# Optimization experiments

Hardware: AMD Instinct MI355X
Metric: run time of the kernel (lower is better)

## Reference

```python
import jax, jax.numpy as jnp
import numpy as np

MAX_DEPTH = 9
HIDDEN = 64
EMB = 64
POS_FREQS = 6
IN_C = 1
SIZES = [4 ** d for d in range(MAX_DEPTH + 1)]
OFFSETS = np.concatenate([[0], np.cumsum(SIZES)])  # per-depth slices into concatenated node arrays
TOTAL = int(OFFSETS[-1])  # 349525
POS_DIM = 3 + 2 * POS_FREQS * 3  # 39


def _interleave(v):
    v = v & 0xFFFF
    v = (v | (v << 8)) & 0x00FF00FF
    v = (v | (v << 4)) & 0x0F0F0F0F
    v = (v | (v << 2)) & 0x33333333
    v = (v | (v << 1)) & 0x55555555
    return v


def _deinterleave(v):
    v = v & 0x55555555
    v = (v | (v >> 1)) & 0x33333333
    v = (v | (v >> 2)) & 0x0F0F0F0F
    v = (v | (v >> 4)) & 0x00FF00FF
    v = (v | (v >> 8)) & 0x0000FFFF
    return v


def _xy(d):
    keys = jnp.arange(4 ** d, dtype=jnp.int32)  # full tree: sorted Morton keys = arange
    return _deinterleave(keys), _deinterleave(keys >> 1)


def _neighbors(d):
    # [N, 9] neighbor indices in Morton order grid; -1 outside the image (matches quadtree.neighs padding)
    ix, iy = _xy(d)
    res = 1 << d
    cols = []
    for dy in (-1, 0, 1):
        for dx in (-1, 0, 1):
            nx, ny = ix + dx, iy + dy
            valid = (nx >= 0) & (nx < res) & (ny >= 0) & (ny < res)
            key = _interleave(nx) | (_interleave(ny) << 1)
            cols.append(jnp.where(valid, key, -1))
    return jnp.stack(cols, axis=1)


def _pos_enc(d):
    # node_centers_from_keys + fourier_encode
    ix, iy = _xy(d)
    res = float(1 << d)
    x = (ix.astype(jnp.float32) + 0.5) / res
    y = (iy.astype(jnp.float32) + 0.5) / res
    dn = jnp.full_like(x, float(d) / float(MAX_DEPTH))
    pos = jnp.stack([x, y, dn], axis=1)  # [N, 3]
    freqs = 2.0 ** jnp.arange(POS_FREQS, dtype=jnp.float32)
    ang = pos[:, :, None] * (2.0 * np.pi) * freqs  # [N, 3, F]
    enc = jnp.concatenate([jnp.sin(ang), jnp.cos(ang)], axis=-1).reshape(pos.shape[0], -1)  # [N, 3*2F]
    return jnp.concatenate([pos, enc], axis=1)  # [N, 39]


def setup_inputs() -> dict:
    key = jax.random.key(0)
    ks = jax.random.split(key, 10)
    s = 0.05
    return {
        "features_in": jax.random.normal(ks[0], (TOTAL, IN_C), jnp.float32),
        "in_proj_W": jax.random.normal(ks[1], (IN_C + POS_DIM, HIDDEN), jnp.float32) * s,
        "in_proj_b": jnp.zeros((HIDDEN,), jnp.float32),
        "conv_W": jax.random.normal(ks[2], (MAX_DEPTH + 1, 9 * HIDDEN, HIDDEN), jnp.float32) * s,
        "conv_b": jnp.zeros((MAX_DEPTH + 1, HIDDEN), jnp.float32),
        "emb_W": jax.random.normal(ks[3], (MAX_DEPTH + 1, HIDDEN, EMB), jnp.float32) * s,
        "emb_b": jnp.zeros((MAX_DEPTH + 1, EMB), jnp.float32),
        "ln_g": jnp.ones((MAX_DEPTH + 1, EMB), jnp.float32),
        "ln_b": jnp.zeros((MAX_DEPTH + 1, EMB), jnp.float32),
        "depth_gain": jnp.ones((MAX_DEPTH + 1,), jnp.float32),
    }


def reference(features_in, in_proj_W, in_proj_b, conv_W, conv_b, emb_W, emb_b, ln_g, ln_b, depth_gain):
    D = MAX_DEPTH
    # per-depth input projection with fourier positional encoding
    h = []
    for d in range(D + 1):
        f = features_in[OFFSETS[d]:OFFSETS[d + 1]]
        x = jnp.concatenate([f, _pos_enc(d)], axis=1)  # [N_d, in_c + 39]
        h.append(x @ in_proj_W + in_proj_b)
    # bottom-up: QuadPool (mean over 4 children; full tree => children of parent i are 4i..4i+3) + QuadConv
    for d in range(D, 0, -1):
        Np = 4 ** (d - 1)
        pooled = h[d].reshape(Np, 4, HIDDEN).mean(axis=1)
        hd1 = h[d - 1] + pooled
        if d - 1 >= 1:
            neigh = _neighbors(d - 1)  # [N, 9], -1 at borders
            N = neigh.shape[0]
            padded = jnp.concatenate([hd1, jnp.zeros((1, HIDDEN), hd1.dtype)], axis=0)
            gi = jnp.where(neigh < 0, N, neigh)
            col = padded[gi].reshape(N, 9 * HIDDEN)
            hd1 = jax.nn.relu(col @ conv_W[d - 1] + conv_b[d - 1])
        h[d - 1] = hd1
    # per-depth embedding head: Linear -> LayerNorm -> depth gain
    outs = []
    eps = 1e-5
    for d in range(D + 1):
        z = h[d] @ emb_W[d] + emb_b[d]
        mu = z.mean(-1, keepdims=True)
        var = ((z - mu) ** 2).mean(-1, keepdims=True)
        z = (z - mu) / jnp.sqrt(var + eps) * ln_g[d] + ln_b[d]
        outs.append(depth_gain[d] * z)
    return jnp.concatenate(outs, axis=0)  # [TOTAL, EMB] (E[0]..E[max_depth] concatenated)
```

## Files before the change

### kernel.cpp

```cpp
#include <hip/hip_runtime.h>
#include <hip/hip_bf16.h>

static constexpr int TOTAL = 349525;
static constexpr int OFFS[11] = {0,1,5,21,85,341,1365,5461,21845,87381,349525};
static constexpr size_t CONV_USH = (size_t)8*9*2*4*64*8;
static constexpr size_t EMB_USH  = (size_t)10*2*4*64*8;
static constexpr size_t FRAG_USH = CONV_USH + EMB_USH;
static constexpr size_t FRAG_BYTES = FRAG_USH*2*2;
static constexpr size_t HPRE_BYTES = (size_t)(87381-85)*64*4;
static constexpr int WPREP_BLOCKS = 164;
static constexpr int INPROJ_BLOCKS = (TOTAL + 127)/128;

typedef __attribute__((ext_vector_type(8))) short short8;
typedef __attribute__((ext_vector_type(4))) float f32x4;

__device__ __forceinline__ unsigned deint(unsigned v){
  v &= 0x55555555u;
  v = (v | (v>>1)) & 0x33333333u;
  v = (v | (v>>2)) & 0x0F0F0F0Fu;
  v = (v | (v>>4)) & 0x00FF00FFu;
  v = (v | (v>>8)) & 0x0000FFFFu;
  return v;
}
__device__ __forceinline__ unsigned ileave(unsigned v){
  v &= 0xFFFFu;
  v = (v | (v<<8)) & 0x00FF00FFu;
  v = (v | (v<<4)) & 0x0F0F0F0Fu;
  v = (v | (v<<2)) & 0x33333333u;
  v = (v | (v<<1)) & 0x55555555u;
  return v;
}
__device__ __forceinline__ unsigned short f2bh(float x){
  unsigned u = __float_as_uint(x);
  return (unsigned short)((u + 0x7FFFu + ((u>>16)&1u)) >> 16);
}
__device__ __forceinline__ float bh2f(unsigned short h){
  return __uint_as_float(((unsigned)h) << 16);
}
__device__ __forceinline__ void split8(float4 a, float4 b, short8 &hi, short8 &lo){
  float v[8] = {a.x,a.y,a.z,a.w,b.x,b.y,b.z,b.w};
  unsigned short hv[8], lv[8];
  #pragma unroll
  for (int j=0;j<8;++j){ hv[j]=f2bh(v[j]); lv[j]=f2bh(v[j]-bh2f(hv[j])); }
  hi = short8{(short)hv[0],(short)hv[1],(short)hv[2],(short)hv[3],
              (short)hv[4],(short)hv[5],(short)hv[6],(short)hv[7]};
  lo = short8{(short)lv[0],(short)lv[1],(short)lv[2],(short)lv[3],
              (short)lv[4],(short)lv[5],(short)lv[6],(short)lv[7]};
}

__global__ __launch_bounds__(256) void k_prep(const float* __restrict__ convW,
    const float* __restrict__ embW,
    unsigned short* __restrict__ WH, unsigned short* __restrict__ WLo,
    const float* __restrict__ feat, const float* __restrict__ ipW,
    const float* __restrict__ ipB, float* __restrict__ h,
    float* __restrict__ hpre){
  __shared__ float Alt[128][44];
  __shared__ float Wl[40][68];
  int t = threadIdx.x;
  if ((int)blockIdx.x < WPREP_BLOCKS){
    int tid = blockIdx.x*256 + t;
    if (tid >= 41984) return;
    const float* src;
    size_t dst;
    if (tid < 36864){
      int l=tid&63, cb=(tid>>6)&3, ks=(tid>>8)&1;
      int x=tid>>9; int m=x%9, Lp=x/9;
      int k0=ks*32+((l>>4)<<3), ch=cb*16+(l&15);
      src = convW + (size_t)(Lp+1)*36864 + (size_t)(m*64+k0)*64 + ch;
      dst = (size_t)tid*8;
    } else {
      int t2 = tid - 36864;
      int l=t2&63, cb=(t2>>6)&3, ks=(t2>>8)&1, d=t2>>9;
      int k0=ks*32+((l>>4)<<3), ch=cb*16+(l&15);
      src = embW + (size_t)d*4096 + (size_t)k0*64 + ch;
      dst = CONV_USH + (size_t)t2*8;
    }
    unsigned short hv[8], lv[8];
    #pragma unroll
    for (int j=0;j<8;++j){
      float v = src[(size_t)j*64];
      unsigned short hh = f2bh(v);
      hv[j] = hh;
      lv[j] = f2bh(v - bh2f(hh));
    }
    short8 vh = {(short)hv[0],(short)hv[1],(short)hv[2],(short)hv[3],
                 (short)hv[4],(short)hv[5],(short)hv[6],(short)hv[7]};
    short8 vl = {(short)lv[0],(short)lv[1],(short)lv[2],(short)lv[3],
                 (short)lv[4],(short)lv[5],(short)lv[6],(short)lv[7]};
    *(short8*)(WH  + dst) = vh;
    *(short8*)(WLo + dst) = vl;
    return;
  }
  int base = ((int)blockIdx.x - WPREP_BLOCKS) * 128;
  for (int idx = t; idx < 40*64; idx += 256)
    Wl[idx >> 6][idx & 63] = ipW[idx];
  if (t < 128){
    int g = base + t;
    float* row = Alt[t];
    if (g < TOTAL){
      int d = 0;
      #pragma unroll
      for (int i = 1; i <= 9; ++i) if (g >= OFFS[i]) d = i;
      int local = g - OFFS[d];
      unsigned ix = deint((unsigned)local), iy = deint(((unsigned)local) >> 1);
      float inv = 1.0f / (float)(1 << d);
      float px = ((float)ix + 0.5f) * inv;
      float py = ((float)iy + 0.5f) * inv;
      float pd = (float)d * (1.0f/9.0f);
      row[0] = feat[g]; row[1] = px; row[2] = py; row[3] = pd;
      float p3[3] = {px, py, pd};
      #pragma unroll
      for (int c = 0; c < 3; ++c){
        float s, co;
        __sincosf(6.28318530717958647692f * p3[c], &s, &co);
        float* rb = row + 4 + c*12;
        #pragma unroll
        for (int f = 0; f < 6; ++f){
          rb[f] = s; rb[6+f] = co;
          float s2 = 2.f*s*co, c2 = 1.f - 2.f*s*s;
          s = s2; co = c2;
        }
      }
    } else {
      #pragma unroll
      for (int k = 0; k < 40; ++k) row[k] = 0.f;
    }
  }
  __syncthreads();
  int tr = t >> 3, tc = t & 7;
  float acc[4][8];
  #pragma unroll
  for (int i=0;i<4;++i)
    #pragma unroll
    for (int c=0;c<8;++c) acc[i][c] = 0.f;
  #pragma unroll 2
  for (int k4 = 0; k4 < 10; ++k4){
    float av4[4][4];
    #pragma unroll
    for (int i=0;i<4;++i){
      float4 aa = *(const float4*)&Alt[tr*4+i][k4*4];
      av4[i][0]=aa.x; av4[i][1]=aa.y; av4[i][2]=aa.z; av4[i][3]=aa.w;
    }
    #pragma unroll
    for (int j=0;j<4;++j){
      float4 lo = *(const float4*)&Wl[k4*4+j][tc*8];
      float4 hi = *(const float4*)&Wl[k4*4+j][tc*8+4];
      float wv[8];
      wv[0]=lo.x; wv[1]=lo.y; wv[2]=lo.z; wv[3]=lo.w;
      wv[4]=hi.x; wv[5]=hi.y; wv[6]=hi.z; wv[7]=hi.w;
      #pragma unroll
      for (int i=0;i<4;++i){
        float a = av4[i][j];
        #pragma unroll
        for (int c=0;c<8;++c) acc[i][c] += a*wv[c];
      }
    }
  }
  #pragma unroll
  for (int i=0;i<4;++i){
    int g = base + tr*4 + i;
    if (g >= TOTAL) continue;
    float ov[8];
    #pragma unroll
    for (int c=0;c<8;++c) ov[c] = acc[i][c] + ipB[tc*8+c];
    float* dst = &h[(size_t)g*64 + tc*8];
    *(float4*)dst       = *(const float4*)&ov[0];
    *(float4*)(dst + 4) = *(const float4*)&ov[4];
    if (hpre && g >= OFFS[4] && g < OFFS[9]){
      float* dp = hpre + (size_t)(g - OFFS[4])*64 + tc*8;
      *(float4*)dp       = *(const float4*)&ov[0];
      *(float4*)(dp + 4) = *(const float4*)&ov[4];
    }
  }
}

__device__ __forceinline__ void conv_dev(float* __restrict__ h,
    const float* __restrict__ hPar,
    const unsigned short* __restrict__ WHl, const unsigned short* __restrict__ WLl,
    const float* __restrict__ Bb, int N, int offL, int offC, int lbits, int bnum,
    unsigned short* haloH, unsigned short* haloL, int* hkey, int t){
  int nb = bnum * 64;
  int res = 1 << lbits;
  if (t < 100){
    int i = t % 10, j = t / 10;
    int gx = (int)deint((unsigned)nb) - 1 + i;
    int gy = (int)deint(((unsigned)nb)>>1) - 1 + j;
    bool ok = (gx>=0 && gy>=0 && gx<res && gy<res);
    hkey[t] = ok ? (int)(ileave((unsigned)gx) | (ileave((unsigned)gy)<<1)) : -1;
  }
  __syncthreads();
  const float* hC = h + (size_t)offC*64;
  for (int e = t; e < 1600; e += 256){
    int hi_ = e >> 4, u = e & 15;
    int key = hkey[hi_];
    float4 r = make_float4(0.f,0.f,0.f,0.f);
    if (key >= 0){
      const float4* c = (const float4*)(hC + (size_t)(4*key)*64) + u;
      float4 c0 = c[0], c1 = c[16], c2 = c[32], c3 = c[48];
      float4 pr = *((const float4*)(hPar + (size_t)key*64) + u);
      r.x = 0.25f*(c0.x+c1.x+c2.x+c3.x) + pr.x;
      r.y = 0.25f*(c0.y+c1.y+c2.y+c3.y) + pr.y;
      r.z = 0.25f*(c0.z+c1.z+c2.z+c3.z) + pr.z;
      r.w = 0.25f*(c0.w+c1.w+c2.w+c3.w) + pr.w;
    }
    unsigned short h0=f2bh(r.x), h1=f2bh(r.y), h2=f2bh(r.z), h3=f2bh(r.w);
    *(ushort4*)&haloH[hi_*72 + u*4] = make_ushort4(h0,h1,h2,h3);
    *(ushort4*)&haloL[hi_*72 + u*4] = make_ushort4(
        f2bh(r.x - bh2f(h0)), f2bh(r.y - bh2f(h1)),
        f2bh(r.z - bh2f(h2)), f2bh(r.w - bh2f(h3)));
  }
  __syncthreads();
  int cb   = __builtin_amdgcn_readfirstlane(t >> 6);
  int lane = t & 63;
  int q = lane >> 4;
  int chl = cb*16 + (lane & 15);
  int lx0,ly0,lx1,ly1,lx2,ly2,lx3,ly3;
  {
    int n0 = (lane&15), n1 = 16+(lane&15), n2 = 32+(lane&15), n3 = 48+(lane&15);
    lx0=(int)deint((unsigned)n0); ly0=(int)deint(((unsigned)n0)>>1);
    lx1=(int)deint((unsigned)n1); ly1=(int)deint(((unsigned)n1)>>1);
    lx2=(int)deint((unsigned)n2); ly2=(int)deint(((unsigned)n2)>>1);
    lx3=(int)deint((unsigned)n3); ly3=(int)deint(((unsigned)n3)>>1);
  }
  f32x4 acc0 = {0.f,0.f,0.f,0.f}, acc1 = acc0, acc2 = acc0, acc3 = acc0;
  #pragma unroll 1
  for (int dy=0;dy<3;++dy){
    #pragma unroll 1
    for (int dx=0;dx<3;++dx){
      int m = dy*3 + dx;
      int r0 = (ly0+dy)*10 + lx0+dx;
      int r1 = (ly1+dy)*10 + lx1+dx;
      int r2 = (ly2+dy)*10 + lx2+dx;
      int r3 = (ly3+dy)*10 + lx3+dx;
      #pragma unroll
      for (int ks=0;ks<2;++ks){
        const unsigned short* fp = WHl + ((size_t)((m*2+ks)*4 + cb)*64 + lane)*8;
        const unsigned short* fq = WLl + ((size_t)((m*2+ks)*4 + cb)*64 + lane)*8;
        short8 bh = *(const short8*)fp;
        short8 bl = *(const short8*)fq;
        int so = (ks*4 + q)*8;
        short8 ah0 = *(const short8*)&haloH[r0*72 + so];
        short8 al0 = *(const short8*)&haloL[r0*72 + so];
        short8 ah1 = *(const short8*)&haloH[r1*72 + so];
        short8 al1 = *(const short8*)&haloL[r1*72 + so];
        short8 ah2 = *(const short8*)&haloH[r2*72 + so];
        short8 al2 = *(const short8*)&haloL[r2*72 + so];
        short8 ah3 = *(const short8*)&haloH[r3*72 + so];
        short8 al3 = *(const short8*)&haloL[r3*72 + so];
        acc0 = __builtin_amdgcn_mfma_f32_16x16x32_bf16(ah0, bh, acc0, 0,0,0);
        acc1 = __builtin_amdgcn_mfma_f32_16x16x32_bf16(ah1, bh, acc1, 0,0,0);
        acc2 = __builtin_amdgcn_mfma_f32_16x16x32_bf16(ah2, bh, acc2, 0,0,0);
        acc3 = __builtin_amdgcn_mfma_f32_16x16x32_bf16(ah3, bh, acc3, 0,0,0);
        acc0 = __builtin_amdgcn_mfma_f32_16x16x32_bf16(al0, bh, acc0, 0,0,0);
        acc1 = __builtin_amdgcn_mfma_f32_16x16x32_bf16(al1, bh, acc1, 0,0,0);
        acc2 = __builtin_amdgcn_mfma_f32_16x16x32_bf16(al2, bh, acc2, 0,0,0);
        acc3 = __builtin_amdgcn_mfma_f32_16x16x32_bf16(al3, bh, acc3, 0,0,0);
        acc0 = __builtin_amdgcn_mfma_f32_16x16x32_bf16(ah0, bl, acc0, 0,0,0);
        acc1 = __builtin_amdgcn_mfma_f32_16x16x32_bf16(ah1, bl, acc1, 0,0,0);
        acc2 = __builtin_amdgcn_mfma_f32_16x16x32_bf16(ah2, bl, acc2, 0,0,0);
        acc3 = __builtin_amdgcn_mfma_f32_16x16x32_bf16(ah3, bl, acc3, 0,0,0);
      }
    }
  }
  float bias = Bb[chl];
  int rowb = q*4;
  float* hO = h + (size_t)(offL + nb)*64;
  #pragma unroll
  for (int reg=0;reg<4;++reg){
    int n0 = rowb + reg;
    float v0 = acc0[reg] + bias; if (nb + n0      < N) hO[(size_t)(n0     )*64 + chl] = v0 > 0.f ? v0 : 0.f;
    float v1 = acc1[reg] + bias; if (nb + n0 + 16 < N) hO[(size_t)(n0 + 16)*64 + chl] = v1 > 0.f ? v1 : 0.f;
    float v2 = acc2[reg] + bias; if (nb + n0 + 32 < N) hO[(size_t)(n0 + 32)*64 + chl] = v2 > 0.f ? v2 : 0.f;
    float v3 = acc3[reg] + bias; if (nb + n0 + 48 < N) hO[(size_t)(n0 + 48)*64 + chl] = v3 > 0.f ? v3 : 0.f;
  }
}

__global__ __launch_bounds__(256) void k_conv(float* __restrict__ h,
    const float* __restrict__ hPar,
    const unsigned short* __restrict__ WHl, const unsigned short* __restrict__ WLl,
    const float* __restrict__ Bb, int N, int offL, int offC, int lbits){
  __shared__ unsigned short haloH[100*72];
  __shared__ unsigned short haloL[100*72];
  __shared__ int hkey[100];
  conv_dev(h, hPar, WHl, WLl, Bb, N, offL, offC, lbits, blockIdx.x,
           haloH, haloL, hkey, threadIdx.x);
}

__device__ __forceinline__ void emb_tile(float* __restrict__ h,
    const unsigned short* __restrict__ EH, const unsigned short* __restrict__ ELo,
    const float* __restrict__ embB, const float* __restrict__ lng,
    const float* __restrict__ lnb, const float* __restrict__ gain,
    int d, size_t rowbase, int validN, int lane){
  int q = lane >> 4, li = lane & 15;
  const float* rp = h + (rowbase + li)*64 + q*8;
  float4 a0 = *(const float4*)rp;
  float4 a1 = *(const float4*)(rp + 4);
  float4 a2 = *(const float4*)(rp + 32);
  float4 a3 = *(const float4*)(rp + 36);
  short8 ah0, al0, ah1, al1;
  split8(a0, a1, ah0, al0);
  split8(a2, a3, ah1, al1);
  f32x4 acc0 = {0.f,0.f,0.f,0.f}, acc1 = acc0, acc2 = acc0, acc3 = acc0;
  #define EMB_CB(CB, ACC) { \
    size_t f0 = (((size_t)(d*2+0)*4 + (CB))*64 + lane)*8; \
    size_t f1 = (((size_t)(d*2+1)*4 + (CB))*64 + lane)*8; \
    short8 bh0 = *(const short8*)(EH + f0); \
    short8 bl0 = *(const short8*)(ELo + f0); \
    short8 bh1 = *(const short8*)(EH + f1); \
    short8 bl1 = *(const short8*)(ELo + f1); \
    ACC = __builtin_amdgcn_mfma_f32_16x16x32_bf16(ah0, bh0, ACC, 0,0,0); \
    ACC = __builtin_amdgcn_mfma_f32_16x16x32_bf16(al0, bh0, ACC, 0,0,0); \
    ACC = __builtin_amdgcn_mfma_f32_16x16x32_bf16(ah0, bl0, ACC, 0,0,0); \
    ACC = __builtin_amdgcn_mfma_f32_16x16x32_bf16(ah1, bh1, ACC, 0,0,0); \
    ACC = __builtin_amdgcn_mfma_f32_16x16x32_bf16(al1, bh1, ACC, 0,0,0); \
    ACC = __builtin_amdgcn_mfma_f32_16x16x32_bf16(ah1, bl1, ACC, 0,0,0); }
  EMB_CB(0, acc0)
  EMB_CB(1, acc1)
  EMB_CB(2, acc2)
  EMB_CB(3, acc3)
  #undef EMB_CB
  float b0 = embB[d*64 +      li];
  float b1 = embB[d*64 + 16 + li];
  float b2 = embB[d*64 + 32 + li];
  float b3 = embB[d*64 + 48 + li];
  float mu[4], rs[4];
  float z0[4], z1[4], z2[4], z3[4];
  #pragma unroll
  for (int r=0;r<4;++r){
    z0[r] = acc0[r] + b0;
    z1[r] = acc1[r] + b1;
    z2[r] = acc2[r] + b2;
    z3[r] = acc3[r] + b3;
    float s  = z0[r] + z1[r] + z2[r] + z3[r];
    float qv = z0[r]*z0[r] + z1[r]*z1[r] + z2[r]*z2[r] + z3[r]*z3[r];
    #pragma unroll
    for (int mk=1; mk<16; mk<<=1){
      s  += __shfl_xor(s, mk, 64);
      qv += __shfl_xor(qv, mk, 64);
    }
    float m = s * 0.015625f;
    mu[r] = m;
    rs[r] = rsqrtf(qv * 0.015625f - m*m + 1e-5f);
  }
  float g0 = lng[d*64 +      li], l0 = lnb[d*64 +      li];
  float g1 = lng[d*64 + 16 + li], l1 = lnb[d*64 + 16 + li];
  float g2 = lng[d*64 + 32 + li], l2 = lnb[d*64 + 32 + li];
  float g3 = lng[d*64 + 48 + li], l3 = lnb[d*64 + 48 + li];
  float gn = gain[d];
  #pragma unroll
  for (int r=0;r<4;++r){
    int ni = q*4 + r;
    if (ni < validN){
      float* row = h + (rowbase + ni)*64;
      row[     li] = ((z0[r] - mu[r])*rs[r]*g0 + l0)*gn;
      row[16 + li] = ((z1[r] - mu[r])*rs[r]*g1 + l1)*gn;
      row[32 + li] = ((z2[r] - mu[r])*rs[r]*g2 + l2)*gn;
      row[48 + li] = ((z3[r] - mu[r])*rs[r]*g3 + l3)*gn;
    }
  }
}
__device__ __forceinline__ void emb128(float* h,
    const unsigned short* EH, const unsigned short* ELo, const float* embB,
    const float* lng, const float* lnb, const float* gain,
    int d, int blk, int t){
  int w = t >> 6, lane = t & 63;
  size_t base = (size_t)OFFS[d] + (size_t)blk*128;
  emb_tile(h, EH, ELo, embB, lng, lnb, gain, d, base + (size_t)w*16,      16, lane);
  emb_tile(h, EH, ELo, embB, lng, lnb, gain, d, base + (size_t)(w+4)*16, 16, lane);
}

template<int L>
__device__ __forceinline__ void tail_level256(float* __restrict__ h,
    const unsigned short* __restrict__ WHc, const unsigned short* __restrict__ WLc,
    const float* __restrict__ convB, const float* __restrict__ Hpar,
    unsigned short* __restrict__ PtH, unsigned short* __restrict__ PtL, int t){
  constexpr int Np  = 1 << (2*L);
  constexpr int NTt = (Np + 15)/16;
  constexpr int res = 1 << L;
  int cb = __builtin_amdgcn_readfirstlane(t >> 6);
  int lane = t & 63;
  int q = lane >> 4, li = lane & 15;
  int chl = cb*16 + li;
  int lx[NTt], ly[NTt];
  #pragma unroll
  for (int i=0;i<NTt;++i){
    unsigned n = (unsigned)(i*16 + li);
    lx[i] = (int)deint(n); ly[i] = (int)deint(n >> 1);
  }
  f32x4 acc[NTt];
  #pragma unroll
  for (int i=0;i<NTt;++i) acc[i] = f32x4{0.f,0.f,0.f,0.f};
  short8 bh0, bl0, bh1, bl1;
  {
    size_t f0 = ((size_t)(0*4 + cb)*64 + lane)*8;
    size_t f1 = ((size_t)(1*4 + cb)*64 + lane)*8;
    bh0 = *(const short8*)(WHc + f0); bl0 = *(const short8*)(WLc + f0);
    bh1 = *(const short8*)(WHc + f1); bl1 = *(const short8*)(WLc + f1);
  }
  #pragma unroll 1
  for (int m=0;m<9;++m){
    short8 nh0, nl0, nh1, nl1;
    if (m < 8){
      size_t f0 = ((size_t)(((m+1)*2+0)*4 + cb)*64 + lane)*8;
      size_t f1 = ((size_t)(((m+1)*2+1)*4 + cb)*64 + lane)*8;
      nh0 = *(const short8*)(WHc + f0); nl0 = *(const short8*)(WLc + f0);
      nh1 = *(const short8*)(WHc + f1); nl1 = *(const short8*)(WLc + f1);
    }
    int dy = m/3 - 1, dx = m%3 - 1;
    #pragma unroll
    for (int i=0;i<NTt;++i){
      int nx = lx[i]+dx, ny = ly[i]+dy;
      int key = (nx>=0 && ny>=0 && nx<res && ny<res)
              ? (int)(ileave((unsigned)nx) | (ileave((unsigned)ny)<<1)) : Np;
      const unsigned short* pH = PtH + key*72;
      const unsigned short* pL = PtL + key*72;
      short8 ah0 = *(const short8*)(pH + q*8);
      short8 al0 = *(const short8*)(pL + q*8);
      short8 ah1 = *(const short8*)(pH + 32 + q*8);
      short8 al1 = *(const short8*)(pL + 32 + q*8);
      acc[i] = __builtin_amdgcn_mfma_f32_16x16x32_bf16(ah0, bh0, acc[i], 0,0,0);
      acc[i] = __builtin_amdgcn_mfma_f32_16x16x32_bf16(al0, bh0, acc[i], 0,0,0);
      acc[i] = __builtin_amdgcn_mfma_f32_16x16x32_bf16(ah0, bl0, acc[i], 0,0,0);
      acc[i] = __builtin_amdgcn_mfma_f32_16x16x32_bf16(ah1, bh1, acc[i], 0,0,0);
      acc[i] = __builtin_amdgcn_mfma_f32_16x16x32_bf16(al1, bh1, acc[i], 0,0,0);
      acc[i] = __builtin_amdgcn_mfma_f32_16x16x32_bf16(ah1, bl1, acc[i], 0,0,0);
    }
    if (m < 8){ bh0 = nh0; bl0 = nl0; bh1 = nh1; bl1 = nl1; }
  }
  float bias = convB[L*64 + chl];
  float vq[NTt][4];
  #pragma unroll
  for (int i=0;i<NTt;++i){
    #pragma unroll
    for (int reg=0;reg<4;++reg){
      int ni = i*16 + q*4 + reg;
      float v = acc[i][reg] + bias;
      v = v > 0.f ? v : 0.f;
      vq[i][reg] = v;
      if (ni < Np) h[(size_t)(OFFS[L] + ni)*64 + chl] = v;
    }
  }
  __syncthreads();
  if (L > 1){
    constexpr int Pp = Np/4;
    #pragma unroll
    for (int i=0;i<NTt;++i){
      int p = i*4 + q;
      if (p < Pp){
        float pooled = 0.25f*(vq[i][0]+vq[i][1]+vq[i][2]+vq[i][3])
                     + Hpar[(size_t)(OFFS[L-1] + p)*64 + chl];
        unsigned short hh = f2bh(pooled);
        PtH[p*72 + chl] = hh;
        PtL[p*72 + chl] = f2bh(pooled - bh2f(hh));
      }
    }
    if (t < 64){ PtH[Pp*72 + t] = 0; PtL[Pp*72 + t] = 0; }
  } else {
    if (q == 0){
      float pooled = 0.25f*(vq[0][0]+vq[0][1]+vq[0][2]+vq[0][3]) + Hpar[chl];
      h[chl] = pooled;
    }
  }
  __syncthreads();
}

__device__ __forceinline__ void do_tail_phase(int b, float* __restrict__ h,
    const unsigned short* WH, const unsigned short* WLo, const float* convB,
    const unsigned short* EH, const unsigned short* ELo, const float* embB,
    const float* lng, const float* lnb, const float* gain,
    unsigned short* PtH, unsigned short* PtL, float* Hpar, int t){
  int w = t >> 6, lane = t & 63;
  if (b != 0){
    if (b < 9) emb128(h, EH, ELo, embB, lng, lnb, gain, 5, b-1, t);
    return;
  }
  for (int e = t; e < 21*16; e += 256)
    ((float4*)Hpar)[e] = ((const float4*)h)[e];
  for (int e = t; e < 65*16; e += 256){
    int node = e >> 4, u = e & 15;
    float4 r = make_float4(0.f,0.f,0.f,0.f);
    if (node < 64){
      const float4* c = (const float4*)(h + (size_t)(OFFS[4] + 4*node)*64) + u;
      float4 c0 = c[0], c1 = c[16], c2 = c[32], c3 = c[48];
      float4 pr = *((const float4*)(h + (size_t)(OFFS[3] + node)*64) + u);
      r.x = 0.25f*(c0.x+c1.x+c2.x+c3.x) + pr.x;
      r.y = 0.25f*(c0.y+c1.y+c2.y+c3.y) + pr.y;
      r.z = 0.25f*(c0.z+c1.z+c2.z+c3.z) + pr.z;
      r.w = 0.25f*(c0.w+c1.w+c2.w+c3.w) + pr.w;
    }
    unsigned short h0=f2bh(r.x), h1=f2bh(r.y), h2=f2bh(r.z), h3=f2bh(r.w);
    *(ushort4*)&PtH[node*72 + u*4] = make_ushort4(h0,h1,h2,h3);
    *(ushort4*)&PtL[node*72 + u*4] = make_ushort4(
        f2bh(r.x - bh2f(h0)), f2bh(r.y - bh2f(h1)),
        f2bh(r.z - bh2f(h2)), f2bh(r.w - bh2f(h3)));
  }
  __syncthreads();
  tail_level256<3>(h, WH + (size_t)2*36864, WLo + (size_t)2*36864, convB, Hpar, PtH, PtL, t);
  tail_level256<2>(h, WH + (size_t)1*36864, WLo + (size_t)1*36864, convB, Hpar, PtH, PtL, t);
  tail_level256<1>(h, WH,                   WLo,                   convB, Hpar, PtH, PtL, t);
  for (int j = w; j < 23; j += 4){
    int d, tile;
    if (j < 16)      { d=4; tile=j;    }
    else if (j < 20) { d=3; tile=j-16; }
    else if (j == 20){ d=2; tile=0;    }
    else if (j == 21){ d=1; tile=0;    }
    else             { d=0; tile=0;    }
    int Nlev = 1 << (2*d);
    int valid = Nlev - tile*16;
    emb_tile(h, EH, ELo, embB, lng, lnb, gain, d,
             (size_t)OFFS[d] + (size_t)tile*16, valid > 16 ? 16 : valid, lane);
  }
}

__global__ __launch_bounds__(256) void k_final(float* __restrict__ h,
    const unsigned short* __restrict__ WH, const unsigned short* __restrict__ WLo,
    const float* __restrict__ convB,
    const unsigned short* __restrict__ EH, const unsigned short* __restrict__ ELo,
    const float* __restrict__ embB, const float* __restrict__ lng,
    const float* __restrict__ lnb, const float* __restrict__ gain){
  __shared__ __align__(16) char smem[24128];
  unsigned short* PtH = (unsigned short*)smem;
  unsigned short* PtL = (unsigned short*)(smem + 9360);
  float* Hpar = (float*)(smem + 18720);
  int t = threadIdx.x;
  int b = blockIdx.x;
  if (b >= 9){
    int bb = b - 9;
    int d, blk;
    if      (bb < 2048){ d = 9; blk = bb;        }
    else if (bb < 2560){ d = 8; blk = bb - 2048; }
    else if (bb < 2688){ d = 7; blk = bb - 2560; }
    else               { d = 6; blk = bb - 2688; }
    emb128(h, EH, ELo, embB, lng, lnb, gain, d, blk, t);
    return;
  }
  do_tail_phase(b, h, WH, WLo, convB, EH, ELo, embB, lng, lnb, gain,
                PtH, PtL, Hpar, t);
}

extern "C" void kernel_launch(void* const* d_in, const int* in_sizes, int n_in,
                              void* d_out, int out_size, void* d_ws, size_t ws_size,
                              hipStream_t stream) {
  (void)in_sizes; (void)n_in; (void)out_size;
  const float* feat  = (const float*)d_in[0];
  const float* ipW   = (const float*)d_in[1];
  const float* ipB   = (const float*)d_in[2];
  const float* convW = (const float*)d_in[3];
  const float* convB = (const float*)d_in[4];
  const float* embW  = (const float*)d_in[5];
  const float* embB  = (const float*)d_in[6];
  const float* lng   = (const float*)d_in[7];
  const float* lnb   = (const float*)d_in[8];
  const float* gain  = (const float*)d_in[9];
  float* h = (float*)d_out;

  unsigned short* WH  = (unsigned short*)d_ws;
  unsigned short* WLo = WH + FRAG_USH;
  const unsigned short* EH  = WH  + CONV_USH;
  const unsigned short* ELo = WLo + CONV_USH;
  float* hpre = (ws_size >= FRAG_BYTES + HPRE_BYTES)
              ? (float*)((char*)d_ws + FRAG_BYTES) : nullptr;

  k_prep<<<WPREP_BLOCKS + INPROJ_BLOCKS, 256, 0, stream>>>(
      convW, embW, WH, WLo, feat, ipW, ipB, h, hpre);

  for (int L = 8; L >= 4; --L){
    int Np = 1 << (2*L);
    const float* hPar = hpre ? (hpre + (size_t)(OFFS[L] - OFFS[4])*64)
                             : (h + (size_t)OFFS[L]*64);
    k_conv<<<Np/64, 256, 0, stream>>>(h, hPar,
        WH  + (size_t)(L-1)*36864, WLo + (size_t)(L-1)*36864,
        convB + (size_t)L*64, Np, OFFS[L], OFFS[L+1], L);
  }

  k_final<<<9 + 2720, 256, 0, stream>>>(h, WH, WLo, convB,
      EH, ELo, embB, lng, lnb, gain);
}
```

Before: 193.3 us.

## Use 1024-thread final blocks with paired embedding tiles and split tail conv

k_final now launches 683 blocks of 1024 threads instead of 2729 blocks of 256. Each embedding wave handles two 16-row tiles at once through a new emb_pair routine, which interleaves MFMAs across independent accumulators and computes LayerNorm with shuffle reductions. The sequential tail block (levels 3..1) now spreads its tiles across 16 waves instead of 4, which shortens the serial critical path of block 0. In exchange the larger blocks and extra accumulators raise per-wave register pressure and may lower occupancy. Depth-5 embedding now runs in regular blocks instead of inside the tail phase.

```diff
diff --git a/kernel.cpp b/kernel.cpp
--- a/kernel.cpp
+++ b/kernel.cpp
@@ -359,37 +359,112 @@
     }
   }
 }
-__device__ __forceinline__ void emb128(float* h,
-    const unsigned short* EH, const unsigned short* ELo, const float* embB,
-    const float* lng, const float* lnb, const float* gain,
-    int d, int blk, int t){
-  int w = t >> 6, lane = t & 63;
-  size_t base = (size_t)OFFS[d] + (size_t)blk*128;
-  emb_tile(h, EH, ELo, embB, lng, lnb, gain, d, base + (size_t)w*16,      16, lane);
-  emb_tile(h, EH, ELo, embB, lng, lnb, gain, d, base + (size_t)(w+4)*16, 16, lane);
+
+__device__ __forceinline__ void emb_pair(float* __restrict__ h,
+    const unsigned short* __restrict__ EH, const unsigned short* __restrict__ ELo,
+    const float* __restrict__ embB, const float* __restrict__ lng,
+    const float* __restrict__ lnb, const float* __restrict__ gain,
+    int d, size_t rb1, size_t rb2, int lane){
+  int q = lane >> 4, li = lane & 15;
+  const float* rp1 = h + (rb1 + li)*64 + q*8;
+  const float* rp2 = h + (rb2 + li)*64 + q*8;
+  float4 x0 = *(const float4*)rp1;
+  float4 x1 = *(const float4*)(rp1 + 4);
+  float4 x2 = *(const float4*)(rp1 + 32);
+  float4 x3 = *(const float4*)(rp1 + 36);
+  float4 y0 = *(const float4*)rp2;
+  float4 y1 = *(const float4*)(rp2 + 4);
+  float4 y2 = *(const float4*)(rp2 + 32);
+  float4 y3 = *(const float4*)(rp2 + 36);
+  short8 Xh0, Xl0, Xh1, Xl1, Yh0, Yl0, Yh1, Yl1;
+  split8(x0, x1, Xh0, Xl0);
+  split8(x2, x3, Xh1, Xl1);
+  split8(y0, y1, Yh0, Yl0);
+  split8(y2, y3, Yh1, Yl1);
+  f32x4 pA0 = {0.f,0.f,0.f,0.f}, pA1 = pA0, pA2 = pA0, pA3 = pA0;
+  f32x4 pB0 = pA0, pB1 = pA0, pB2 = pA0, pB3 = pA0;
+  #define EMB_CB2(CB, ACCA, ACCB) { \
+    size_t f0 = (((size_t)(d*2+0)*4 + (CB))*64 + lane)*8; \
+    size_t f1 = (((size_t)(d*2+1)*4 + (CB))*64 + lane)*8; \
+    short8 bh0 = *(const short8*)(EH + f0); \
+    short8 bl0 = *(const short8*)(ELo + f0); \
+    short8 bh1 = *(const short8*)(EH + f1); \
+    short8 bl1 = *(const short8*)(ELo + f1); \
+    ACCA = __builtin_amdgcn_mfma_f32_16x16x32_bf16(Xh0, bh0, ACCA, 0,0,0); \
+    ACCB = __builtin_amdgcn_mfma_f32_16x16x32_bf16(Yh0, bh0, ACCB, 0,0,0); \
+    ACCA = __builtin_amdgcn_mfma_f32_16x16x32_bf16(Xl0, bh0, ACCA, 0,0,0); \
+    ACCB = __builtin_amdgcn_mfma_f32_16x16x32_bf16(Yl0, bh0, ACCB, 0,0,0); \
+    ACCA = __builtin_amdgcn_mfma_f32_16x16x32_bf16(Xh0, bl0, ACCA, 0,0,0); \
+    ACCB = __builtin_amdgcn_mfma_f32_16x16x32_bf16(Yh0, bl0, ACCB, 0,0,0); \
+    ACCA = __builtin_amdgcn_mfma_f32_16x16x32_bf16(Xh1, bh1, ACCA, 0,0,0); \
+    ACCB = __builtin_amdgcn_mfma_f32_16x16x32_bf16(Yh1, bh1, ACCB, 0,0,0); \
+    ACCA = __builtin_amdgcn_mfma_f32_16x16x32_bf16(Xl1, bh1, ACCA, 0,0,0); \
+    ACCB = __builtin_amdgcn_mfma_f32_16x16x32_bf16(Yl1, bh1, ACCB, 0,0,0); \
+    ACCA = __builtin_amdgcn_mfma_f32_16x16x32_bf16(Xh1, bl1, ACCA, 0,0,0); \
+    ACCB = __builtin_amdgcn_mfma_f32_16x16x32_bf16(Yh1, bl1, ACCB, 0,0,0); }
+  EMB_CB2(0, pA0, pB0)
+  EMB_CB2(1, pA1, pB1)
+  EMB_CB2(2, pA2, pB2)
+  EMB_CB2(3, pA3, pB3)
+  #undef EMB_CB2
+  float b0 = embB[d*64 +      li];
+  float b1 = embB[d*64 + 16 + li];
+  float b2 = embB[d*64 + 32 + li];
+  float b3 = embB[d*64 + 48 + li];
+  float g0 = lng[d*64 +      li], l0 = lnb[d*64 +      li];
+  float g1 = lng[d*64 + 16 + li], l1 = lnb[d*64 + 16 + li];
+  float g2 = lng[d*64 + 32 + li], l2 = lnb[d*64 + 32 + li];
+  float g3 = lng[d*64 + 48 + li], l3 = lnb[d*64 + 48 + li];
+  float gn = gain[d];
+  #define EMB_FIN(ACC0, ACC1, ACC2, ACC3, RB) { \
+    _Pragma("unroll") \
+    for (int r=0;r<4;++r){ \
+      float z0 = ACC0[r] + b0, z1 = ACC1[r] + b1; \
+      float z2 = ACC2[r] + b2, z3 = ACC3[r] + b3; \
+      float s  = z0 + z1 + z2 + z3; \
+      float qv = z0*z0 + z1*z1 + z2*z2 + z3*z3; \
+      _Pragma("unroll") \
+      for (int mk=1; mk<16; mk<<=1){ \
+        s  += __shfl_xor(s, mk, 64); \
+        qv += __shfl_xor(qv, mk, 64); \
+      } \
+      float m = s * 0.015625f; \
+      float rsv = rsqrtf(qv * 0.015625f - m*m + 1e-5f); \
+      float* row = h + ((RB) + (size_t)(q*4 + r))*64; \
+      row[     li] = ((z0 - m)*rsv*g0 + l0)*gn; \
+      row[16 + li] = ((z1 - m)*rsv*g1 + l1)*gn; \
+      row[32 + li] = ((z2 - m)*rsv*g2 + l2)*gn; \
+      row[48 + li] = ((z3 - m)*rsv*g3 + l3)*gn; \
+    } }
+  EMB_FIN(pA0, pA1, pA2, pA3, rb1)
+  EMB_FIN(pB0, pB1, pB2, pB3, rb2)
+  #undef EMB_FIN
 }
 
 template<int L>
-__device__ __forceinline__ void tail_level256(float* __restrict__ h,
+__device__ __forceinline__ void tail_level2(float* __restrict__ h,
     const unsigned short* __restrict__ WHc, const unsigned short* __restrict__ WLc,
     const float* __restrict__ convB, const float* __restrict__ Hpar,
     unsigned short* __restrict__ PtH, unsigned short* __restrict__ PtL, int t){
   constexpr int Np  = 1 << (2*L);
   constexpr int NTt = (Np + 15)/16;
+  constexpr int TG  = (NTt + 3)/4;
   constexpr int res = 1 << L;
-  int cb = __builtin_amdgcn_readfirstlane(t >> 6);
+  int w  = t >> 6;
+  int cb = __builtin_amdgcn_readfirstlane(w & 3);
+  int tg = __builtin_amdgcn_readfirstlane(w >> 2);
   int lane = t & 63;
   int q = lane >> 4, li = lane & 15;
   int chl = cb*16 + li;
-  int lx[NTt], ly[NTt];
-  #pragma unroll
-  for (int i=0;i<NTt;++i){
-    unsigned n = (unsigned)(i*16 + li);
+  int lx[TG], ly[TG];
+  #pragma unroll
+  for (int i=0;i<TG;++i){
+    unsigned n = (unsigned)((tg*TG + i)*16 + li);
     lx[i] = (int)deint(n); ly[i] = (int)deint(n >> 1);
   }
-  f32x4 acc[NTt];
-  #pragma unroll
-  for (int i=0;i<NTt;++i) acc[i] = f32x4{0.f,0.f,0.f,0.f};
+  f32x4 acc[TG];
+  #pragma unroll
+  for (int i=0;i<TG;++i) acc[i] = f32x4{0.f,0.f,0.f,0.f};
   short8 bh0, bl0, bh1, bl1;
   {
     size_t f0 = ((size_t)(0*4 + cb)*64 + lane)*8;
@@ -408,7 +483,7 @@
     }
     int dy = m/3 - 1, dx = m%3 - 1;
     #pragma unroll
-    for (int i=0;i<NTt;++i){
+    for (int i=0;i<TG;++i){
       int nx = lx[i]+dx, ny = ly[i]+dy;
       int key = (nx>=0 && ny>=0 && nx<res && ny<res)
               ? (int)(ileave((unsigned)nx) | (ileave((unsigned)ny)<<1)) : Np;
@@ -428,12 +503,12 @@
     if (m < 8){ bh0 = nh0; bl0 = nl0; bh1 = nh1; bl1 = nl1; }
   }
   float bias = convB[L*64 + chl];
-  float vq[NTt][4];
-  #pragma unroll
-  for (int i=0;i<NTt;++i){
+  float vq[TG][4];
+  #pragma unroll
+  for (int i=0;i<TG;++i){
     #pragma unroll
     for (int reg=0;reg<4;++reg){
-      int ni = i*16 + q*4 + reg;
+      int ni = (tg*TG + i)*16 + q*4 + reg;
       float v = acc[i][reg] + bias;
       v = v > 0.f ? v : 0.f;
       vq[i][reg] = v;
@@ -444,8 +519,8 @@
   if (L > 1){
     constexpr int Pp = Np/4;
     #pragma unroll
-    for (int i=0;i<NTt;++i){
-      int p = i*4 + q;
+    for (int i=0;i<TG;++i){
+      int p = (tg*TG + i)*4 + q;
       if (p < Pp){
         float pooled = 0.25f*(vq[i][0]+vq[i][1]+vq[i][2]+vq[i][3])
                      + Hpar[(size_t)(OFFS[L-1] + p)*64 + chl];
@@ -456,7 +531,7 @@
     }
     if (t < 64){ PtH[Pp*72 + t] = 0; PtL[Pp*72 + t] = 0; }
   } else {
-    if (q == 0){
+    if (tg == 0 && q == 0){
       float pooled = 0.25f*(vq[0][0]+vq[0][1]+vq[0][2]+vq[0][3]) + Hpar[chl];
       h[chl] = pooled;
     }
@@ -464,19 +539,35 @@
   __syncthreads();
 }
 
-__device__ __forceinline__ void do_tail_phase(int b, float* __restrict__ h,
-    const unsigned short* WH, const unsigned short* WLo, const float* convB,
-    const unsigned short* EH, const unsigned short* ELo, const float* embB,
-    const float* lng, const float* lnb, const float* gain,
-    unsigned short* PtH, unsigned short* PtL, float* Hpar, int t){
+__global__ __launch_bounds__(1024) void k_final(float* __restrict__ h,
+    const unsigned short* __restrict__ WH, const unsigned short* __restrict__ WLo,
+    const float* __restrict__ convB,
+    const unsigned short* __restrict__ EH, const unsigned short* __restrict__ ELo,
+    const float* __restrict__ embB, const float* __restrict__ lng,
+    const float* __restrict__ lnb, const float* __restrict__ gain){
+  __shared__ __align__(16) char smem[24128];
+  unsigned short* PtH = (unsigned short*)smem;
+  unsigned short* PtL = (unsigned short*)(smem + 9360);
+  float* Hpar = (float*)(smem + 18720);
+  int t = threadIdx.x;
   int w = t >> 6, lane = t & 63;
+  int b = blockIdx.x;
   if (b != 0){
-    if (b < 9) emb128(h, EH, ELo, embB, lng, lnb, gain, 5, b-1, t);
+    int bb = b - 1;
+    int d, blk;
+    if      (bb < 512){ d = 9; blk = bb;       }
+    else if (bb < 640){ d = 8; blk = bb - 512; }
+    else if (bb < 672){ d = 7; blk = bb - 640; }
+    else if (bb < 680){ d = 6; blk = bb - 672; }
+    else              { d = 5; blk = bb - 680; }
+    size_t base = (size_t)OFFS[d] + (size_t)blk*512;
+    emb_pair(h, EH, ELo, embB, lng, lnb, gain, d,
+             base + (size_t)w*16, base + (size_t)(w+16)*16, lane);
     return;
   }
-  for (int e = t; e < 21*16; e += 256)
+  for (int e = t; e < 21*16; e += 1024)
     ((float4*)Hpar)[e] = ((const float4*)h)[e];
-  for (int e = t; e < 65*16; e += 256){
+  for (int e = t; e < 65*16; e += 1024){
     int node = e >> 4, u = e & 15;
     float4 r = make_float4(0.f,0.f,0.f,0.f);
     if (node < 64){
@@ -495,10 +586,10 @@
         f2bh(r.z - bh2f(h2)), f2bh(r.w - bh2f(h3)));
   }
   __syncthreads();
-  tail_level256<3>(h, WH + (size_t)2*36864, WLo + (size_t)2*36864, convB, Hpar, PtH, PtL, t);
-  tail_level256<2>(h, WH + (size_t)1*36864, WLo + (size_t)1*36864, convB, Hpar, PtH, PtL, t);
-  tail_level256<1>(h, WH,                   WLo,                   convB, Hpar, PtH, PtL, t);
-  for (int j = w; j < 23; j += 4){
+  tail_level2<3>(h, WH + (size_t)2*36864, WLo + (size_t)2*36864, convB, Hpar, PtH, PtL, t);
+  tail_level2<2>(h, WH + (size_t)1*36864, WLo + (size_t)1*36864, convB, Hpar, PtH, PtL, t);
+  tail_level2<1>(h, WH,                   WLo,                   convB, Hpar, PtH, PtL, t);
+  for (int j = w; j < 23; j += 16){
     int d, tile;
     if (j < 16)      { d=4; tile=j;    }
     else if (j < 20) { d=3; tile=j-16; }
@@ -510,32 +601,6 @@
     emb_tile(h, EH, ELo, embB, lng, lnb, gain, d,
              (size_t)OFFS[d] + (size_t)tile*16, valid > 16 ? 16 : valid, lane);
   }
-}
-
-__global__ __launch_bounds__(256) void k_final(float* __restrict__ h,
-    const unsigned short* __restrict__ WH, const unsigned short* __restrict__ WLo,
-    const float* __restrict__ convB,
-    const unsigned short* __restrict__ EH, const unsigned short* __restrict__ ELo,
-    const float* __restrict__ embB, const float* __restrict__ lng,
-    const float* __restrict__ lnb, const float* __restrict__ gain){
-  __shared__ __align__(16) char smem[24128];
-  unsigned short* PtH = (unsigned short*)smem;
-  unsigned short* PtL = (unsigned short*)(smem + 9360);
-  float* Hpar = (float*)(smem + 18720);
-  int t = threadIdx.x;
-  int b = blockIdx.x;
-  if (b >= 9){
-    int bb = b - 9;
-    int d, blk;
-    if      (bb < 2048){ d = 9; blk = bb;        }
-    else if (bb < 2560){ d = 8; blk = bb - 2048; }
-    else if (bb < 2688){ d = 7; blk = bb - 2560; }
-    else               { d = 6; blk = bb - 2688; }
-    emb128(h, EH, ELo, embB, lng, lnb, gain, d, blk, t);
-    return;
-  }
-  do_tail_phase(b, h, WH, WLo, convB, EH, ELo, embB, lng, lnb, gain,
-                PtH, PtL, Hpar, t);
 }
 
 extern "C" void kernel_launch(void* const* d_in, const int* in_sizes, int n_in,
@@ -573,6 +638,6 @@
         convB + (size_t)L*64, Np, OFFS[L], OFFS[L+1], L);
   }
 
-  k_final<<<9 + 2720, 256, 0, stream>>>(h, WH, WLo, convB,
+  k_final<<<1 + 682, 1024, 0, stream>>>(h, WH, WLo, convB,
       EH, ELo, embB, lng, lnb, gain);
 }
```

Measured after the change: 180.8 us (median of 2 runs). -6.5%, faster.
